# Kernel tuning notes

Hardware: AMD Instinct MI355X
Metric: run time of the kernel (lower is better)

## Reference

```python
import jax, jax.numpy as jnp
import numpy as np

B, S, D = 2, 1024, 4096
H, KVH = 32, 8
HD = D // H          # 128
N_REP = H // KVH     # 4
R = 2                # LoRA rank


def setup_inputs() -> dict:
    key = jax.random.key(0)
    ks = jax.random.split(key, 10)
    sc = 0.02
    x = jax.random.normal(ks[0], (B, S, D), jnp.float32)
    wq = jax.random.normal(ks[1], (D, H * HD), jnp.float32) * sc
    wk = jax.random.normal(ks[2], (D, KVH * HD), jnp.float32) * sc
    wv = jax.random.normal(ks[3], (D, KVH * HD), jnp.float32) * sc
    wo = jax.random.normal(ks[4], (H * HD, D), jnp.float32) * sc
    lora_q_a = jax.random.normal(ks[5], (D, R), jnp.float32) * sc
    lora_q_b = jax.random.normal(ks[6], (R, H * HD), jnp.float32) * sc
    lora_v_a = jax.random.normal(ks[7], (D, R), jnp.float32) * sc
    lora_v_b = jax.random.normal(ks[8], (R, KVH * HD), jnp.float32) * sc
    # RoPE frequencies: freqs_cis[t, i] = exp(1j * t * 10000^(-2i/HD))
    inv_freq = 1.0 / (10000.0 ** (jnp.arange(0, HD, 2, dtype=jnp.float32) / HD))  # [HD/2]
    t = jnp.arange(S, dtype=jnp.float32)
    ang = jnp.outer(t, inv_freq)                      # [S, HD/2]
    freqs_cos = jnp.cos(ang)
    freqs_sin = jnp.sin(ang)
    # causal additive mask [1, 1, S, S]
    mask = jnp.triu(jnp.full((S, S), -1e9, jnp.float32), k=1)[None, None]
    return {"x": x, "wq": wq, "wk": wk, "wv": wv, "wo": wo,
            "lora_q_a": lora_q_a, "lora_q_b": lora_q_b,
            "lora_v_a": lora_v_a, "lora_v_b": lora_v_b,
            "freqs_cos": freqs_cos, "freqs_sin": freqs_sin,
            "mask": mask, "start_pos": 0}


def _rope(t, cos, sin):
    # t: [B, S, h, HD]; pairs (even, odd) are (real, imag) of complex halves
    b, s, h, hd = t.shape
    tr = t.reshape(b, s, h, hd // 2, 2)
    a, bb = tr[..., 0], tr[..., 1]
    c = cos[None, :, None, :]
    sn = sin[None, :, None, :]
    out = jnp.stack([a * c - bb * sn, a * sn + bb * c], axis=-1)
    return out.reshape(b, s, h, hd)


def reference(x, wq, wk, wv, wo, lora_q_a, lora_q_b, lora_v_a, lora_v_b,
              freqs_cos, freqs_sin, mask, start_pos):
    # projections + LoRA (note: original Lora_layer applies NO scaling in forward)
    xq = x @ wq + (x @ lora_q_a) @ lora_q_b            # [B,S,H*HD]
    xk = x @ wk                                         # [B,S,KVH*HD]
    xv = x @ wv + (x @ lora_v_a) @ lora_v_b             # [B,S,KVH*HD]
    xq = xq.reshape(B, S, H, HD)
    xk = xk.reshape(B, S, KVH, HD)
    xv = xv.reshape(B, S, KVH, HD)
    xq = _rope(xq, freqs_cos, freqs_sin)
    xk = _rope(xk, freqs_cos, freqs_sin)
    # repeat_kv (GQA expansion): [B,S,KVH,HD] -> [B,S,H,HD]
    k = jnp.repeat(xk, N_REP, axis=2)
    v = jnp.repeat(xv, N_REP, axis=2)
    # attention
    scores = jnp.einsum('bshd,bthd->bhst', xq, k) / np.sqrt(HD).astype(np.float32)
    scores = scores + mask
    probs = jax.nn.softmax(scores.astype(jnp.float32), axis=-1).astype(xq.dtype)
    out = jnp.einsum('bhst,bthd->bshd', probs, v)       # [B,S,H,HD]
    out = out.reshape(B, S, H * HD) @ wo                # [B,S,D]
    return out
```

## Files before the change

### kernel.cpp

```cpp
#include <hip/hip_runtime.h>
#include <stdint.h>

#define B_ 2
#define S_ 1024
#define D_ 4096
#define H_ 32
#define KVH_ 8
#define HD_ 128

typedef short short8 __attribute__((ext_vector_type(8)));
typedef float floatx4 __attribute__((ext_vector_type(4)));

__device__ __forceinline__ ushort f2bf(float f) {
  union { float f; uint32_t u; } v; v.f = f;
  return (ushort)((v.u + 0x7FFFu + ((v.u >> 16) & 1u)) >> 16);
}
__device__ __forceinline__ float bf2f(ushort u) {
  union { uint32_t x; float f; } v; v.x = ((uint32_t)u) << 16; return v.f;
}

__device__ __forceinline__ void gload16(const void* g, void* l) {
  __builtin_amdgcn_global_load_lds((__attribute__((address_space(1))) void*)g,
                                   (__attribute__((address_space(3))) void*)l,
                                   16, 0, 0);
}

__global__ __launch_bounds__(256) void k_cvtlora(const float* __restrict__ x,
                                                 const float* __restrict__ qa,
                                                 const float* __restrict__ va,
                                                 ushort* __restrict__ xb,
                                                 float* __restrict__ xa) {
  const int row = blockIdx.x, t = threadIdx.x;
  const float* xr = x + (size_t)row * D_;
  ushort* xo = xb + (size_t)row * D_;
  float a0 = 0, a1 = 0, a2 = 0, a3 = 0;
#pragma unroll
  for (int it = 0; it < 4; it++) {
    const int i = it * 1024 + t * 4;
    float4 v = *(const float4*)(xr + i);
    ushort o4[4] = {f2bf(v.x), f2bf(v.y), f2bf(v.z), f2bf(v.w)};
    *(uint2*)(xo + i) = *(uint2*)o4;
    float4 q0 = *(const float4*)(qa + 2 * i);
    float4 q1 = *(const float4*)(qa + 2 * i + 4);
    float4 w0 = *(const float4*)(va + 2 * i);
    float4 w1 = *(const float4*)(va + 2 * i + 4);
    a0 += v.x * q0.x + v.y * q0.z + v.z * q1.x + v.w * q1.z;
    a1 += v.x * q0.y + v.y * q0.w + v.z * q1.y + v.w * q1.w;
    a2 += v.x * w0.x + v.y * w0.z + v.z * w1.x + v.w * w1.z;
    a3 += v.x * w0.y + v.y * w0.w + v.z * w1.y + v.w * w1.w;
  }
#pragma unroll
  for (int off = 32; off; off >>= 1) {
    a0 += __shfl_down(a0, off, 64);
    a1 += __shfl_down(a1, off, 64);
    a2 += __shfl_down(a2, off, 64);
    a3 += __shfl_down(a3, off, 64);
  }
  __shared__ float red[4][4];
  const int w = t >> 6, lane = t & 63;
  if (lane == 0) { red[w][0] = a0; red[w][1] = a1; red[w][2] = a2; red[w][3] = a3; }
  __syncthreads();
  if (t < 4)
    xa[(size_t)row * 4 + t] = red[0][t] + red[1][t] + red[2][t] + red[3][t];
}

__global__ __launch_bounds__(256) void k_trw2(const float* __restrict__ in0,
                                              const float* __restrict__ in1,
                                              ushort* __restrict__ out0,
                                              ushort* __restrict__ out1,
                                              int in_stride, int out_stride) {
  const float* in = blockIdx.z ? in1 : in0;
  ushort* out = blockIdx.z ? out1 : out0;
  __shared__ float t[64][65];
  const int n0 = blockIdx.x * 64, k0 = blockIdx.y * 64;
  const int c4 = (threadIdx.x & 15) * 4, r = threadIdx.x >> 4;
#pragma unroll
  for (int rr = 0; rr < 64; rr += 16) {
    float4 v = *(const float4*)&in[(size_t)(k0 + r + rr) * in_stride + n0 + c4];
    t[r + rr][c4] = v.x; t[r + rr][c4 + 1] = v.y;
    t[r + rr][c4 + 2] = v.z; t[r + rr][c4 + 3] = v.w;
  }
  __syncthreads();
#pragma unroll
  for (int rr = 0; rr < 64; rr += 16) {
    const int n = r + rr;
    ushort o4[4] = {f2bf(t[c4][n]), f2bf(t[c4 + 1][n]),
                    f2bf(t[c4 + 2][n]), f2bf(t[c4 + 3][n])};
    *(uint2*)&out[(size_t)(n0 + n) * out_stride + k0 + c4] = *(uint2*)o4;
  }
}

#define GBAR __builtin_amdgcn_s_barrier()
#define VMCNT0 asm volatile("s_waitcnt vmcnt(0)" ::: "memory")
#define VMCNT4 asm volatile("s_waitcnt vmcnt(4)" ::: "memory")
#define VMCNT6 asm volatile("s_waitcnt vmcnt(6)" ::: "memory")

#define QSTG(T, SB) do {                                                     \
    const ushort* ga_ = A + (size_t)(m0 + srow) * Kz + (T) * 32 + ssl;       \
    gload16(ga_, qlds + (SB) * 32768 + w * 1024);                            \
    _Pragma("unroll") for (int u_ = 0; u_ < 3; u_++) {                       \
      const ushort* gb_ = Bt + (size_t)(n0 + u_ * 128 + srow) * Kz + (T) * 32 + ssl; \
      gload16(gb_, qlds + (SB) * 32768 + 8192 + u_ * 8192 + w * 1024);       \
    }                                                                        \
  } while (0)

#define QTILE(T, RB) do {                                                    \
    if ((T) + 2 < 128) QSTG((T) + 2, ((RB) + 2) % 3);                        \
    const char* ab_ = qlds + (RB) * 32768 + (wr * 64 + lr) * 64 + ((g ^ (lr & 3)) << 4); \
    _Pragma("unroll") for (int fr = 0; fr < 4; fr++)                         \
      af[fr] = *(const short8*)(ab_ + fr * 1024);                            \
    const char* bb_ = qlds + (RB) * 32768 + 8192 + (wc * 32 + lr) * 64 + ((g ^ (lr & 3)) << 4); \
    _Pragma("unroll") for (int u_ = 0; u_ < 3; u_++)                         \
    _Pragma("unroll") for (int e_ = 0; e_ < 2; e_++)                         \
      bfr[u_ * 2 + e_] = *(const short8*)(bb_ + u_ * 8192 + e_ * 1024);      \
    __builtin_amdgcn_s_setprio(1);                                           \
    _Pragma("unroll") for (int fr = 0; fr < 4; fr++)                         \
    _Pragma("unroll") for (int u_ = 0; u_ < 6; u_++)                         \
      acc[fr][u_] = __builtin_amdgcn_mfma_f32_16x16x32_bf16(                 \
          af[fr], bfr[u_], acc[fr][u_], 0, 0, 0);                            \
    __builtin_amdgcn_s_setprio(0);                                           \
    if ((T) + 2 < 128) { VMCNT4; } else { VMCNT0; }                          \
    GBAR;                                                                    \
  } while (0)

__global__ __launch_bounds__(512, 2) void k_gemmq(const ushort* __restrict__ A,
                                                  const ushort* __restrict__ Bt,
                                                  ushort* __restrict__ xq,
                                                  ushort* __restrict__ Vt,
                                                  const float* __restrict__ xa,
                                                  const float* __restrict__ qb,
                                                  const float* __restrict__ vb) {
  __shared__ char qlds[98304];
  const int flat = blockIdx.y * 16 + blockIdx.x;
  const int swz_id = (flat & 7) * 32 + (flat >> 3);
  const int m0 = (swz_id >> 4) * 128, n0 = (swz_id & 15) * 384;
  const int tid = threadIdx.x, lane = tid & 63, w = tid >> 6;
  const int wr = w >> 2, wc = w & 3;
  const int lr = lane & 15, g = lane >> 4;
  const size_t Kz = 4096;
  const int srow = tid >> 2;
  const int ssl = ((tid & 3) ^ (srow & 3)) * 8;

  floatx4 acc[4][6] = {};
  short8 af[4], bfr[6];

  QSTG(0, 0); QSTG(1, 1);
  VMCNT4;
  GBAR;

  for (int tt = 0; tt < 126; tt += 3) {
    QTILE(tt + 0, 0);
    QTILE(tt + 1, 1);
    QTILE(tt + 2, 2);
  }
  QTILE(126, 0);
  QTILE(127, 1);

#pragma unroll
  for (int fr = 0; fr < 4; fr++) {
    const int mb = m0 + wr * 64 + fr * 16 + g * 4;
    const int bb = mb >> 10, s0 = mb & 1023;
    float4 xa4[4];
#pragma unroll
    for (int r = 0; r < 4; r++) xa4[r] = *(const float4*)&xa[(size_t)(mb + r) * 4];
#pragma unroll
    for (int j = 0; j < 3; j++)
#pragma unroll
      for (int e = 0; e < 2; e++) {
        const int n = n0 + j * 128 + wc * 32 + e * 16 + lr;
        if (n < 5120) {
          const bool lq = (n < 4096);
          float b0 = 0.f, b1 = 0.f;
          if (lq) { b0 = qb[n]; b1 = qb[4096 + n]; }
#pragma unroll
          for (int r = 0; r < 4; r++) {
            float cc = acc[fr][j * 2 + e][r];
            if (lq) cc += xa4[r].x * b0 + xa4[r].y * b1;
            xq[(size_t)(mb + r) * 6144 + n] = f2bf(cc);
          }
        } else {
          const int vcol = n - 5120;
          const float b0 = vb[vcol], b1 = vb[1024 + vcol];
          ushort v4[4];
#pragma unroll
          for (int r = 0; r < 4; r++)
            v4[r] = f2bf(acc[fr][j * 2 + e][r] + xa4[r].z * b0 + xa4[r].w * b1);
          *(uint2*)&Vt[(size_t)((bb * 8 + (vcol >> 7)) * 128 + (vcol & 127)) * 1024 + s0] =
              *(uint2*)v4;
        }
      }
  }
}

#define OSTG(T, SB) do {                                                     \
    const ushort* ga_ = A + (size_t)(m0 + w * 16 + osr) * Kz + (T) * 64 + osc; \
    char* la_ = olds + (SB) * 49152 + w * 2048;                              \
    gload16(ga_, la_); gload16(ga_ + 8 * Kz, la_ + 1024);                    \
    _Pragma("unroll") for (int u_ = 0; u_ < 2; u_++) {                       \
      const ushort* gb_ = Bt + (size_t)(n0 + u_ * 128 + w * 16 + osr) * Kz + (T) * 64 + osc; \
      char* lb_ = olds + (SB) * 49152 + 16384 + u_ * 16384 + w * 2048;       \
      gload16(gb_, lb_); gload16(gb_ + 8 * Kz, lb_ + 1024);                  \
    }                                                                        \
  } while (0)

#define OTILE(T, RB) do {                                                    \
    if ((T) + 2 < 64) OSTG((T) + 2, ((RB) + 2) % 3);                         \
    const char* ab_ = olds + (RB) * 49152 + (wr * 64 + lr) * 128;            \
    _Pragma("unroll") for (int fr = 0; fr < 4; fr++)                         \
    _Pragma("unroll") for (int ks = 0; ks < 2; ks++)                         \
      af[fr][ks] = *(const short8*)(ab_ + fr * 2048 + (((ks * 4 + g) * 16) ^ swz)); \
    const char* bb_ = olds + (RB) * 49152 + 16384 + (wc * 32 + lr) * 128;    \
    _Pragma("unroll") for (int u_ = 0; u_ < 2; u_++)                         \
    _Pragma("unroll") for (int e_ = 0; e_ < 2; e_++)                         \
    _Pragma("unroll") for (int ks = 0; ks < 2; ks++)                         \
      bfr[u_ * 2 + e_][ks] = *(const short8*)(bb_ + u_ * 16384 + e_ * 2048 + (((ks * 4 + g) * 16) ^ swz)); \
    __builtin_amdgcn_s_setprio(1);                                           \
    _Pragma("unroll") for (int fr = 0; fr < 4; fr++)                         \
    _Pragma("unroll") for (int u_ = 0; u_ < 4; u_++)                         \
    _Pragma("unroll") for (int ks = 0; ks < 2; ks++)                         \
      acc[fr][u_] = __builtin_amdgcn_mfma_f32_16x16x32_bf16(                 \
          af[fr][ks], bfr[u_][ks], acc[fr][u_], 0, 0, 0);                    \
    __builtin_amdgcn_s_setprio(0);                                           \
    if ((T) + 2 < 64) { VMCNT6; } else { VMCNT0; }                           \
    GBAR;                                                                    \
  } while (0)

__global__ __launch_bounds__(512, 2) void k_gemmo(const ushort* __restrict__ A,
                                                  const ushort* __restrict__ Bt,
                                                  float* __restrict__ C) {
  __shared__ char olds[147456];
  const int flat = blockIdx.y * 16 + blockIdx.x;
  const int swz_id = (flat & 7) * 32 + (flat >> 3);
  const int m0 = (swz_id >> 4) * 128, n0 = (swz_id & 15) * 256;
  const int tid = threadIdx.x, lane = tid & 63, w = tid >> 6;
  const int wr = w >> 2, wc = w & 3;
  const int lr = lane & 15, g = lane >> 4;
  const int swz = (lr & 7) * 16;
  const size_t Kz = 4096;
  const int osr = lane >> 3;
  const int osc = ((lane & 7) ^ (osr & 7)) * 8;

  floatx4 acc[4][4] = {};
  short8 af[4][2], bfr[4][2];

  OSTG(0, 0); OSTG(1, 1);
  VMCNT6;
  GBAR;

  for (int tt = 0; tt < 63; tt += 3) {
    OTILE(tt + 0, 0);
    OTILE(tt + 1, 1);
    OTILE(tt + 2, 2);
  }
  OTILE(63, 0);

#pragma unroll
  for (int fr = 0; fr < 4; fr++) {
    const int mb = m0 + wr * 64 + fr * 16 + g * 4;
#pragma unroll
    for (int j = 0; j < 2; j++)
#pragma unroll
      for (int e = 0; e < 2; e++) {
        const int n = n0 + j * 128 + wc * 32 + e * 16 + lr;
#pragma unroll
        for (int r = 0; r < 4; r++)
          C[(size_t)(mb + r) * 4096 + n] = acc[fr][j * 2 + e][r];
      }
  }
}

__global__ __launch_bounds__(256) void k_rope(const ushort* __restrict__ xq,
                                              const float* __restrict__ fcos,
                                              const float* __restrict__ fsin,
                                              ushort* __restrict__ Qb,
                                              ushort* __restrict__ Kb) {
  const int s = blockIdx.x, b = blockIdx.y;
  const ushort* row = xq + (size_t)(b * S_ + s) * 6144;
#pragma unroll
  for (int it = 0; it < 8; it++) {
    int p2 = it * 256 + threadIdx.x;
    int h = p2 >> 6, p = p2 & 63;
    uint32_t u = *(const uint32_t*)(row + h * 128 + 2 * p);
    float a = bf2f((ushort)u), bb = bf2f((ushort)(u >> 16));
    float c = fcos[s * 64 + p], sn = fsin[s * 64 + p];
    uint32_t pk = (uint32_t)f2bf(a * c - bb * sn) |
                  ((uint32_t)f2bf(a * sn + bb * c) << 16);
    *(uint32_t*)(Qb + ((size_t)(b * H_ + h) * S_ + s) * HD_ + 2 * p) = pk;
  }
#pragma unroll
  for (int it = 0; it < 2; it++) {
    int p2 = it * 256 + threadIdx.x;
    int h = p2 >> 6, p = p2 & 63;
    uint32_t u = *(const uint32_t*)(row + 4096 + h * 128 + 2 * p);
    float a = bf2f((ushort)u), bb = bf2f((ushort)(u >> 16));
    float c = fcos[s * 64 + p], sn = fsin[s * 64 + p];
    uint32_t pk = (uint32_t)f2bf(a * c - bb * sn) |
                  ((uint32_t)f2bf(a * sn + bb * c) << 16);
    *(uint32_t*)(Kb + ((size_t)(b * KVH_ + h) * S_ + s) * HD_ + 2 * p) = pk;
  }
}

#define FSTAGE(T, DB) do {                                                   \
    _Pragma("unroll") for (int i_ = 0; i_ < 4; i_++) {                       \
      gload16(Kg + (size_t)((T) * 64 + i_ * 16 + k_srow) * HD_ + k_scol,     \
              fls + (DB) * 16384 + i_ * 4096 + w * 1024);                    \
      gload16(Vg + (size_t)(i_ * 32 + v_srow) * S_ + (T) * 64 + v_scol,      \
              fls + 32768 + (DB) * 16384 + i_ * 4096 + w * 1024);            \
    }                                                                        \
  } while (0)

__global__ __launch_bounds__(256, 2) void k_flash(const ushort* __restrict__ Qb,
                                                  const ushort* __restrict__ Kb,
                                                  const ushort* __restrict__ Vt,
                                                  ushort* __restrict__ attn) {
  __shared__ char fls[81920];
  const int qblk = (gridDim.x - 1) - blockIdx.x;
  const int h = blockIdx.y, b = blockIdx.z;
  const int kvh = h >> 2;
  const int tid = threadIdx.x, w = tid >> 6, lane = tid & 63;
  const int lr = lane & 15, g = lane >> 4;
  const int swz = (lr & 7) * 16;
  const int qra = qblk * 128 + w * 16;
  const ushort* Qrow = Qb + ((size_t)(b * H_ + h) * S_ + qra + lr) * HD_;
  short8 qfa[4], qfb[4];
#pragma unroll
  for (int ks = 0; ks < 4; ks++) {
    qfa[ks] = *(const short8*)(Qrow + ks * 32 + g * 8);
    qfb[ks] = *(const short8*)(Qrow + 64 * HD_ + ks * 32 + g * 8);
  }
  const ushort* Kg = Kb + (size_t)(b * KVH_ + kvh) * S_ * HD_;
  const ushort* Vg = Vt + (size_t)(b * KVH_ + kvh) * HD_ * S_;
  char* Pw = fls + 65536 + w * 4096;
  const int q7 = lr & 7;
  const int k_srow = tid >> 4;
  const int k_scol = ((tid & 15) ^ (k_srow & 7)) * 8;
  const int v_srow = tid >> 3;
  const int v_scol = ((tid & 7) ^ (v_srow & 7)) * 8;
  const float scale = 0.088388347648318447f;

  float m_a = -1e30f, l_a = 0.f, m_b = -1e30f, l_b = 0.f;
  floatx4 oa[8] = {}, ob[8] = {};
  const int nt = 2 * qblk + 2;
  const int lastA = 2 * qblk;

  FSTAGE(0, 0);
  VMCNT0;
  GBAR;

  for (int t = 0; t < nt; t++) {
    const int cur = t & 1;
    if (t + 1 < nt) FSTAGE(t + 1, cur ^ 1);
    const char* Kl = fls + cur * 16384;
    const char* Vl = fls + 32768 + cur * 16384;
    if (t <= lastA) {
      floatx4 s4[4] = {};
      __builtin_amdgcn_s_setprio(1);
#pragma unroll
      for (int mf = 0; mf < 4; mf++) {
        const char* Krow = Kl + (mf * 16 + lr) * 256;
#pragma unroll
        for (int ks = 0; ks < 4; ks++) {
          short8 kf = *(const short8*)(Krow + (((ks * 4 + g) * 16) ^ swz));
          s4[mf] = __builtin_amdgcn_mfma_f32_16x16x32_bf16(kf, qfa[ks], s4[mf], 0, 0, 0);
        }
      }
      __builtin_amdgcn_s_setprio(0);
      float tm = -1e30f;
      if (t == lastA) {
#pragma unroll
        for (int mf = 0; mf < 4; mf++)
#pragma unroll
          for (int r = 0; r < 4; r++) {
            int kv = t * 64 + mf * 16 + g * 4 + r;
            float v = (kv > qra + lr) ? -1e30f : s4[mf][r] * scale;
            s4[mf][r] = v; tm = fmaxf(tm, v);
          }
      } else {
#pragma unroll
        for (int mf = 0; mf < 4; mf++)
#pragma unroll
          for (int r = 0; r < 4; r++) {
            float v = s4[mf][r] * scale;
            s4[mf][r] = v; tm = fmaxf(tm, v);
          }
      }
      tm = fmaxf(tm, __shfl_xor(tm, 16, 64));
      tm = fmaxf(tm, __shfl_xor(tm, 32, 64));
      float m_new = fmaxf(m_a, tm);
      float corr = __expf(m_a - m_new);
      float rs = 0.f;
#pragma unroll
      for (int mf = 0; mf < 4; mf++)
#pragma unroll
        for (int r = 0; r < 4; r++) {
          float p = __expf(s4[mf][r] - m_new);
          s4[mf][r] = p; rs += p;
        }
      rs += __shfl_xor(rs, 16, 64);
      rs += __shfl_xor(rs, 32, 64);
      l_a = l_a * corr + rs; m_a = m_new;
#pragma unroll
      for (int r = 0; r < 4; r++) {
        float cr = __shfl(corr, g * 4 + r, 64);
#pragma unroll
        for (int nf = 0; nf < 8; nf++) oa[nf][r] *= cr;
      }
#pragma unroll
      for (int mf = 0; mf < 4; mf++) {
        uint2 pv;
        pv.x = (uint32_t)f2bf(s4[mf][0]) | ((uint32_t)f2bf(s4[mf][1]) << 16);
        pv.y = (uint32_t)f2bf(s4[mf][2]) | ((uint32_t)f2bf(s4[mf][3]) << 16);
        *(uint2*)(Pw + lr * 128 + ((mf * 32 + g * 8) ^ (q7 << 4))) = pv;
      }
    }
    {
      floatx4 s4[4] = {};
      __builtin_amdgcn_s_setprio(1);
#pragma unroll
      for (int mf = 0; mf < 4; mf++) {
        const char* Krow = Kl + (mf * 16 + lr) * 256;
#pragma unroll
        for (int ks = 0; ks < 4; ks++) {
          short8 kf = *(const short8*)(Krow + (((ks * 4 + g) * 16) ^ swz));
          s4[mf] = __builtin_amdgcn_mfma_f32_16x16x32_bf16(kf, qfb[ks], s4[mf], 0, 0, 0);
        }
      }
      __builtin_amdgcn_s_setprio(0);
      float tm = -1e30f;
      if (t == nt - 1) {
#pragma unroll
        for (int mf = 0; mf < 4; mf++)
#pragma unroll
          for (int r = 0; r < 4; r++) {
            int kv = t * 64 + mf * 16 + g * 4 + r;
            float v = (kv > qra + 64 + lr) ? -1e30f : s4[mf][r] * scale;
            s4[mf][r] = v; tm = fmaxf(tm, v);
          }
      } else {
#pragma unroll
        for (int mf = 0; mf < 4; mf++)
#pragma unroll
          for (int r = 0; r < 4; r++) {
            float v = s4[mf][r] * scale;
            s4[mf][r] = v; tm = fmaxf(tm, v);
          }
      }
      tm = fmaxf(tm, __shfl_xor(tm, 16, 64));
      tm = fmaxf(tm, __shfl_xor(tm, 32, 64));
      float m_new = fmaxf(m_b, tm);
      float corr = __expf(m_b - m_new);
      float rs = 0.f;
#pragma unroll
      for (int mf = 0; mf < 4; mf++)
#pragma unroll
        for (int r = 0; r < 4; r++) {
          float p = __expf(s4[mf][r] - m_new);
          s4[mf][r] = p; rs += p;
        }
      rs += __shfl_xor(rs, 16, 64);
      rs += __shfl_xor(rs, 32, 64);
      l_b = l_b * corr + rs; m_b = m_new;
#pragma unroll
      for (int r = 0; r < 4; r++) {
        float cr = __shfl(corr, g * 4 + r, 64);
#pragma unroll
        for (int nf = 0; nf < 8; nf++) ob[nf][r] *= cr;
      }
#pragma unroll
      for (int mf = 0; mf < 4; mf++) {
        uint2 pv;
        pv.x = (uint32_t)f2bf(s4[mf][0]) | ((uint32_t)f2bf(s4[mf][1]) << 16);
        pv.y = (uint32_t)f2bf(s4[mf][2]) | ((uint32_t)f2bf(s4[mf][3]) << 16);
        *(uint2*)(Pw + 2048 + lr * 128 + ((mf * 32 + g * 8) ^ (q7 << 4))) = pv;
      }
    }
    __builtin_amdgcn_s_setprio(1);
#pragma unroll
    for (int ks2 = 0; ks2 < 2; ks2++) {
      short8 pb = *(const short8*)(Pw + 2048 + lr * 128 + ((ks2 * 64 + g * 16) ^ (q7 << 4)));
      short8 pa = pb;
      if (t <= lastA)
        pa = *(const short8*)(Pw + lr * 128 + ((ks2 * 64 + g * 16) ^ (q7 << 4)));
#pragma unroll
      for (int nf = 0; nf < 8; nf++) {
        short8 vf = *(const short8*)(Vl + (nf * 16 + lr) * 128 + (((ks2 * 4 + g) * 16) ^ swz));
        if (t <= lastA)
          oa[nf] = __builtin_amdgcn_mfma_f32_16x16x32_bf16(pa, vf, oa[nf], 0, 0, 0);
        ob[nf] = __builtin_amdgcn_mfma_f32_16x16x32_bf16(pb, vf, ob[nf], 0, 0, 0);
      }
    }
    __builtin_amdgcn_s_setprio(0);
    VMCNT0;
    GBAR;
  }
  const float linva = 1.0f / l_a, linvb = 1.0f / l_b;
  ushort* outp = attn + ((size_t)(b * S_) + qra) * 4096 + h * 128;
#pragma unroll
  for (int r = 0; r < 4; r++) {
    float lia = __shfl(linva, g * 4 + r, 64);
    float lib = __shfl(linvb, g * 4 + r, 64);
    ushort* orow = outp + (size_t)(g * 4 + r) * 4096;
#pragma unroll
    for (int nf = 0; nf < 8; nf++) {
      orow[nf * 16 + lr] = f2bf(oa[nf][r] * lia);
      orow[(size_t)64 * 4096 + nf * 16 + lr] = f2bf(ob[nf][r] * lib);
    }
  }
}

extern "C" void kernel_launch(void* const* d_in, const int* in_sizes, int n_in,
                              void* d_out, int out_size, void* d_ws, size_t ws_size,
                              hipStream_t stream) {
  (void)in_sizes; (void)n_in; (void)out_size; (void)ws_size;
  const float* x    = (const float*)d_in[0];
  const float* wq   = (const float*)d_in[1];
  const float* wk   = (const float*)d_in[2];
  const float* wv   = (const float*)d_in[3];
  const float* wo   = (const float*)d_in[4];
  const float* lqa  = (const float*)d_in[5];
  const float* lqb  = (const float*)d_in[6];
  const float* lva  = (const float*)d_in[7];
  const float* lvb  = (const float*)d_in[8];
  const float* fcos = (const float*)d_in[9];
  const float* fsin = (const float*)d_in[10];

  char* ws = (char*)d_ws;
  ushort* xb   = (ushort*)(ws + 0);
  ushort* wT   = (ushort*)(ws + 16777216);
  ushort* woT  = (ushort*)(ws + 67108864);
  ushort* xq   = (ushort*)(ws + 100663296);
  ushort* Qb   = (ushort*)(ws + 150994944);
  ushort* Kb   = (ushort*)(ws + 167772160);
  ushort* Vt   = (ushort*)(ws + 171966464);
  ushort* attn = (ushort*)(ws + 176160768);
  float*  xa   = (float*) (ws + 192937984);

  k_cvtlora<<<2048, 256, 0, stream>>>(x, lqa, lva, xb, xa);
  k_trw2<<<dim3(64, 64, 2), 256, 0, stream>>>(wq, wo, wT, woT, 4096, 4096);
  k_trw2<<<dim3(16, 64, 2), 256, 0, stream>>>(wk, wv, wT + (size_t)4096 * 4096,
                                              wT + (size_t)5120 * 4096, 1024, 4096);
  k_gemmq<<<dim3(16, 16), 512, 0, stream>>>(xb, wT, xq, Vt, xa, lqb, lvb);
  k_rope<<<dim3(1024, 2), 256, 0, stream>>>(xq, fcos, fsin, Qb, Kb);
  k_flash<<<dim3(8, 32, 2), 256, 0, stream>>>(Qb, Kb, Vt, attn);
  k_gemmo<<<dim3(16, 16), 512, 0, stream>>>(attn, woT, (float*)d_out);
}
```

Measured before the change: 308.6 us.

## Fuse RoPE into QKV GEMM epilogue and change LDS swizzle pattern

Removes the separate RoPE kernel by applying the rotation in the QKV GEMM epilogue, pairing even and odd columns through a lane shuffle and writing Q and K straight into head-major layout. This drops the intermediate xq buffer round trip and one kernel launch. The LDS swizzle for staging and fragment reads also changes to XOR with (row>>1)&3, intended to reduce bank conflicts. The epilogue now issues scattered 2-byte stores with a head-dim stride and extra cos/sin loads, which may be less coalesced than before.

```diff
diff --git a/kernel.cpp b/kernel.cpp
--- a/kernel.cpp
+++ b/kernel.cpp
@@ -106,10 +106,10 @@
 
 #define QTILE(T, RB) do {                                                    \
     if ((T) + 2 < 128) QSTG((T) + 2, ((RB) + 2) % 3);                        \
-    const char* ab_ = qlds + (RB) * 32768 + (wr * 64 + lr) * 64 + ((g ^ (lr & 3)) << 4); \
+    const char* ab_ = qlds + (RB) * 32768 + (wr * 64 + lr) * 64 + rswz;      \
     _Pragma("unroll") for (int fr = 0; fr < 4; fr++)                         \
       af[fr] = *(const short8*)(ab_ + fr * 1024);                            \
-    const char* bb_ = qlds + (RB) * 32768 + 8192 + (wc * 32 + lr) * 64 + ((g ^ (lr & 3)) << 4); \
+    const char* bb_ = qlds + (RB) * 32768 + 8192 + (wc * 32 + lr) * 64 + rswz; \
     _Pragma("unroll") for (int u_ = 0; u_ < 3; u_++)                         \
     _Pragma("unroll") for (int e_ = 0; e_ < 2; e_++)                         \
       bfr[u_ * 2 + e_] = *(const short8*)(bb_ + u_ * 8192 + e_ * 1024);      \
@@ -125,11 +125,14 @@
 
 __global__ __launch_bounds__(512, 2) void k_gemmq(const ushort* __restrict__ A,
                                                   const ushort* __restrict__ Bt,
-                                                  ushort* __restrict__ xq,
+                                                  ushort* __restrict__ Qb,
+                                                  ushort* __restrict__ Kb,
                                                   ushort* __restrict__ Vt,
                                                   const float* __restrict__ xa,
                                                   const float* __restrict__ qb,
-                                                  const float* __restrict__ vb) {
+                                                  const float* __restrict__ vb,
+                                                  const float* __restrict__ fcos,
+                                                  const float* __restrict__ fsin) {
   __shared__ char qlds[98304];
   const int flat = blockIdx.y * 16 + blockIdx.x;
   const int swz_id = (flat & 7) * 32 + (flat >> 3);
@@ -139,7 +142,8 @@
   const int lr = lane & 15, g = lane >> 4;
   const size_t Kz = 4096;
   const int srow = tid >> 2;
-  const int ssl = ((tid & 3) ^ (srow & 3)) * 8;
+  const int ssl = ((tid & 3) ^ ((srow >> 1) & 3)) * 8;
+  const int rswz = (g ^ ((lr >> 1) & 3)) << 4;
 
   floatx4 acc[4][6] = {};
   short8 af[4], bfr[6];
@@ -172,11 +176,20 @@
           const bool lq = (n < 4096);
           float b0 = 0.f, b1 = 0.f;
           if (lq) { b0 = qb[n]; b1 = qb[4096 + n]; }
+          const int p = (n & 127) >> 1;
+          const bool even = !(n & 1);
+          const int d = n & 127;
+          ushort* dst = lq ? (Qb + ((size_t)(bb * H_ + (n >> 7)) * S_) * HD_ + d)
+                           : (Kb + ((size_t)(bb * KVH_ + ((n - 4096) >> 7)) * S_) * HD_ + d);
 #pragma unroll
           for (int r = 0; r < 4; r++) {
             float cc = acc[fr][j * 2 + e][r];
             if (lq) cc += xa4[r].x * b0 + xa4[r].y * b1;
-            xq[(size_t)(mb + r) * 6144 + n] = f2bf(cc);
+            float pv = __shfl_xor(cc, 1, 64);
+            const int s = s0 + r;
+            float c = fcos[s * 64 + p], sn = fsin[s * 64 + p];
+            float o = even ? (cc * c - pv * sn) : (cc * c + pv * sn);
+            dst[(size_t)s * HD_] = f2bf(o);
           }
         } else {
           const int vcol = n - 5120;
@@ -269,37 +282,6 @@
   }
 }
 
-__global__ __launch_bounds__(256) void k_rope(const ushort* __restrict__ xq,
-                                              const float* __restrict__ fcos,
-                                              const float* __restrict__ fsin,
-                                              ushort* __restrict__ Qb,
-                                              ushort* __restrict__ Kb) {
-  const int s = blockIdx.x, b = blockIdx.y;
-  const ushort* row = xq + (size_t)(b * S_ + s) * 6144;
-#pragma unroll
-  for (int it = 0; it < 8; it++) {
-    int p2 = it * 256 + threadIdx.x;
-    int h = p2 >> 6, p = p2 & 63;
-    uint32_t u = *(const uint32_t*)(row + h * 128 + 2 * p);
-    float a = bf2f((ushort)u), bb = bf2f((ushort)(u >> 16));
-    float c = fcos[s * 64 + p], sn = fsin[s * 64 + p];
-    uint32_t pk = (uint32_t)f2bf(a * c - bb * sn) |
-                  ((uint32_t)f2bf(a * sn + bb * c) << 16);
-    *(uint32_t*)(Qb + ((size_t)(b * H_ + h) * S_ + s) * HD_ + 2 * p) = pk;
-  }
-#pragma unroll
-  for (int it = 0; it < 2; it++) {
-    int p2 = it * 256 + threadIdx.x;
-    int h = p2 >> 6, p = p2 & 63;
-    uint32_t u = *(const uint32_t*)(row + 4096 + h * 128 + 2 * p);
-    float a = bf2f((ushort)u), bb = bf2f((ushort)(u >> 16));
-    float c = fcos[s * 64 + p], sn = fsin[s * 64 + p];
-    uint32_t pk = (uint32_t)f2bf(a * c - bb * sn) |
-                  ((uint32_t)f2bf(a * sn + bb * c) << 16);
-    *(uint32_t*)(Kb + ((size_t)(b * KVH_ + h) * S_ + s) * HD_ + 2 * p) = pk;
-  }
-}
-
 #define FSTAGE(T, DB) do {                                                   \
     _Pragma("unroll") for (int i_ = 0; i_ < 4; i_++) {                       \
       gload16(Kg + (size_t)((T) * 64 + i_ * 16 + k_srow) * HD_ + k_scol,     \
@@ -528,7 +510,6 @@
   ushort* xb   = (ushort*)(ws + 0);
   ushort* wT   = (ushort*)(ws + 16777216);
   ushort* woT  = (ushort*)(ws + 67108864);
-  ushort* xq   = (ushort*)(ws + 100663296);
   ushort* Qb   = (ushort*)(ws + 150994944);
   ushort* Kb   = (ushort*)(ws + 167772160);
   ushort* Vt   = (ushort*)(ws + 171966464);
@@ -539,8 +520,8 @@
   k_trw2<<<dim3(64, 64, 2), 256, 0, stream>>>(wq, wo, wT, woT, 4096, 4096);
   k_trw2<<<dim3(16, 64, 2), 256, 0, stream>>>(wk, wv, wT + (size_t)4096 * 4096,
                                               wT + (size_t)5120 * 4096, 1024, 4096);
-  k_gemmq<<<dim3(16, 16), 512, 0, stream>>>(xb, wT, xq, Vt, xa, lqb, lvb);
-  k_rope<<<dim3(1024, 2), 256, 0, stream>>>(xq, fcos, fsin, Qb, Kb);
+  k_gemmq<<<dim3(16, 16), 512, 0, stream>>>(xb, wT, Qb, Kb, Vt, xa, lqb, lvb,
+                                            fcos, fsin);
   k_flash<<<dim3(8, 32, 2), 256, 0, stream>>>(Qb, Kb, Vt, attn);
   k_gemmo<<<dim3(16, 16), 512, 0, stream>>>(attn, woT, (float*)d_out);
 }
```

Measured after the change: 293.9 us. -4.7%, faster.
